# Optimization experiments

Hardware: AMD Instinct MI355X
Metric: run time of the kernel (lower is better)

The kernel has to match this reference:

```python
import jax, jax.numpy as jnp
import numpy as np

# ---- static config (mirrors GaussianLSS __init__) ----
ORF_H, ORF_W = 256, 704
FC, FH, FW = 128, 32, 88
D_ST, D_END, D_STEP = 4.0, 45.0, 1.0
OUT_C = 128
ERROR_TOL = 1.0
OPACITY_THR = 0.05
XB = (-50.0, 50.0, 1.0)
YB = (-50.0, 50.0, 1.0)
BEV_H = int(round((YB[1] - YB[0]) / YB[2]))
BEV_W = int(round((XB[1] - XB[0]) / XB[2]))
DS = np.arange(D_ST, D_END, D_STEP, dtype=np.float32)
D = DS.shape[0]  # 41
BN_EPS = 1e-3
CHUNK = 512      # gaussians composited per scan step (16896 = 33*512)
B, NCAM = 1, 6


def make_frustum():
    ds = jnp.broadcast_to(jnp.asarray(DS)[:, None, None], (D, FH, FW))
    xs = jnp.broadcast_to(jnp.linspace(0.0, ORF_W - 1.0, FW)[None, None, :], (D, FH, FW))
    ys = jnp.broadcast_to(jnp.linspace(0.0, ORF_H - 1.0, FH)[None, :, None], (D, FH, FW))
    return jnp.stack([xs, ys, ds], -1)  # [D,FH,FW,3]


def get_geometry(rots, trans, intrins, post_rots, post_trans):
    fr = make_frustum()
    pts = fr[None, None] - post_trans[:, :, None, None, None, :]
    pts = jnp.einsum('bnij,bndhwj->bndhwi', jnp.linalg.inv(post_rots), pts)
    pts = jnp.concatenate([pts[..., :2] * pts[..., 2:3], pts[..., 2:3]], -1)
    comb = jnp.einsum('bnij,bnjk->bnik', rots, jnp.linalg.inv(intrins))
    pts = jnp.einsum('bnij,bndhwj->bndhwi', comb, pts) + trans[:, :, None, None, None, :]
    return pts  # [B,N,D,FH,FW,3] ego-frame frustum points


def conv2d(x, w, b, pad):
    y = jax.lax.conv_general_dilated(x, w, (1, 1), [(pad, pad), (pad, pad)],
                                     dimension_numbers=('NCHW', 'OIHW', 'NCHW'))
    return y + b[None, :, None, None]


def bnorm(x, g, bt, m, v):
    s = (g / jnp.sqrt(v + BN_EPS))[None, :, None, None]
    return (x - m[None, :, None, None]) * s + bt[None, :, None, None]


def splat(means, cov6, colors, ops, valid_in):
    # Differentiable BEV gaussian rasterization (3DGS math, orthographic BEV camera,
    # all depths equal -> compositing in stable gaussian-index order).
    H, W = BEV_H, BEV_W
    sh, sw = H / 2.0, W / 2.0  # h/h_meters with FoV=2 (BEVCamera)
    my = -sh * means[:, 1] + H / 2.0  # pixel row (full_proj_transform row 0)
    mx = -sw * means[:, 0] + W / 2.0  # pixel col (row 1)
    a = sh * sh * cov6[:, 3] + 0.3    # 2D cov = J Sigma_xy J^T, +0.3 low-pass as in 3DGS
    c = sw * sw * cov6[:, 0] + 0.3
    b = sh * sw * cov6[:, 1]
    det = a * c - b * b
    valid = valid_in & (det > 0)
    inv_det = jnp.where(det > 0, 1.0 / det, 0.0)
    cA, cB, cC = c * inv_det, -b * inv_det, a * inv_det
    pi = jnp.repeat(jnp.arange(H, dtype=jnp.float32), W)  # [P] pixel rows
    pj = jnp.tile(jnp.arange(W, dtype=jnp.float32), H)    # [P] pixel cols
    G = means.shape[0]
    nchunk = G // CHUNK
    resh = lambda x: x.reshape((nchunk, CHUNK) + x.shape[1:])
    chunks = (resh(my), resh(mx), resh(cA), resh(cB), resh(cC),
              resh(ops), resh(valid), resh(colors))

    def body(carry, ch):
        logT, acc = carry
        my_c, mx_c, A, Bc, Cc, op_c, val_c, col_c = ch
        dI = pi[None, :] - my_c[:, None]                     # [Gc,P]
        dJ = pj[None, :] - mx_c[:, None]
        q = A[:, None] * dI * dI + 2.0 * Bc[:, None] * dI * dJ + Cc[:, None] * dJ * dJ
        alpha = jnp.minimum(0.99, op_c[:, None] * jnp.exp(-0.5 * q))
        alpha = jnp.where(val_c[:, None] & (q >= 0) & (alpha >= 1.0 / 255.0), alpha, 0.0)
        log1m = jnp.log1p(-alpha)
        cum = jnp.cumsum(log1m, axis=0)
        T = jnp.exp(logT[None, :] + cum - log1m)             # transmittance before each gaussian
        acc = acc + jnp.einsum('gp,gc->pc', alpha * T, col_c)
        return (logT + cum[-1], acc), None

    P = H * W
    init = (jnp.zeros((P,), jnp.float32), jnp.zeros((P, colors.shape[1]), jnp.float32))
    (_, acc), _ = jax.lax.scan(jax.checkpoint(body), init, chunks)
    return acc.reshape(H, W, -1).transpose(2, 0, 1)  # [C,H,W], bg is zeros


def _forward(cam2ego_rot, cam2ego_trans, cam_intrins, post_cam2ego_rot, post_cam2ego_trans,
             img_feats, conv1_w, conv1_b, bn1_g, bn1_b, bn1_m, bn1_v,
             conv2_w, conv2_b, bn2_g, bn2_b, bn2_m, bn2_v, conv3_w, conv3_b):
    geom = get_geometry(cam2ego_rot, cam2ego_trans, cam_intrins, post_cam2ego_rot, post_cam2ego_trans)
    b, n = img_feats.shape[:2]
    x = img_feats.reshape(b * n, FC, FH, FW)
    x = jax.nn.relu(bnorm(conv2d(x, conv1_w, conv1_b, 1), bn1_g, bn1_b, bn1_m, bn1_v))
    x = jax.nn.relu(bnorm(conv2d(x, conv2_w, conv2_b, 1), bn2_g, bn2_b, bn2_m, bn2_v))
    x = conv2d(x, conv3_w, conv3_b, 0)
    depth_prob = jax.nn.softmax(x[:, :D], axis=1).reshape(b, n, D, FH, FW)
    opac = jax.nn.sigmoid(x[:, D:D + 1]).reshape(b, n, FH, FW)
    feats = x[:, D + 1:].reshape(b, n, OUT_C, FH, FW)
    # per-pixel gaussian moments of the depth distribution (compute_gaussian)
    means = jnp.einsum('bndhw,bndhwi->bnhwi', depth_prob, geom)
    delta = means[:, :, None] - geom                                       # [B,N,D,FH,FW,3]
    cov = jnp.einsum('bndhw,bndhwi,bndhwj->bnhwij', depth_prob, delta, delta) * (ERROR_TOL ** 2 / 9.0)
    center = jnp.array([(XB[0] + XB[1]) / 2.0, (YB[0] + YB[1]) / 2.0, 0.0], jnp.float32)
    scale = jnp.array([2.0 / (XB[1] - XB[0]), 2.0 / (YB[1] - YB[0]), 1.0], jnp.float32)
    m_n = (means - center) * scale
    cov_n = cov * (scale[:, None] * scale[None, :])
    cov6 = jnp.stack([cov_n[..., 0, 0], cov_n[..., 0, 1], cov_n[..., 0, 2],
                      cov_n[..., 1, 1], cov_n[..., 1, 2], cov_n[..., 2, 2]], -1)
    g = n * FH * FW
    colors = feats.transpose(0, 1, 3, 4, 2).reshape(b, g, OUT_C)
    m_n = m_n.reshape(b, g, 3)
    cov6 = cov6.reshape(b, g, 6)
    ops = opac.reshape(b, g)
    mask = ops > OPACITY_THR  # opacity filtering == zero contribution, order preserved
    bev = jax.vmap(splat)(m_n, cov6, colors, ops, mask)                    # [B,C,H,W]
    num_gaussians = mask.astype(jnp.float32).sum(-1).mean()
    return bev, num_gaussians


def setup_inputs():
    key = jax.random.key(0)
    ks = jax.random.split(key, 8)
    # camera-to-ego rotations: cam->ego axis permutation composed with per-camera yaw
    yaw = np.linspace(0.0, 2.0 * np.pi, NCAM, endpoint=False).astype(np.float32)
    cz, sz = np.cos(yaw), np.sin(yaw)
    rotz = np.zeros((NCAM, 3, 3), np.float32)
    rotz[:, 0, 0] = cz; rotz[:, 0, 1] = -sz
    rotz[:, 1, 0] = sz; rotz[:, 1, 1] = cz
    rotz[:, 2, 2] = 1.0
    perm = np.array([[0.0, 0.0, 1.0], [-1.0, 0.0, 0.0], [0.0, -1.0, 0.0]], np.float32)
    rots = np.einsum('nij,jk->nik', rotz, perm)
    cam2ego_rot = jnp.asarray(np.broadcast_to(rots, (B, NCAM, 3, 3)).copy())
    cam2ego_trans = jax.random.normal(ks[0], (B, NCAM, 3), jnp.float32)
    K = np.array([[600.0, 0.0, ORF_W / 2.0], [0.0, 600.0, ORF_H / 2.0], [0.0, 0.0, 1.0]], np.float32)
    cam_intrins = jnp.asarray(np.broadcast_to(K, (B, NCAM, 3, 3)).copy())
    post_cam2ego_rot = jnp.broadcast_to(jnp.eye(3, dtype=jnp.float32), (B, NCAM, 3, 3)) + jnp.zeros((B, NCAM, 3, 3), jnp.float32)
    post_cam2ego_trans = jnp.zeros((B, NCAM, 3), jnp.float32)
    img_feats = jax.random.normal(ks[1], (B, NCAM, FC, FH, FW), jnp.float32)
    def conv_init(k, o, i, kh, kw):
        return jax.random.normal(k, (o, i, kh, kw), jnp.float32) * (1.0 / np.sqrt(i * kh * kw))
    return dict(cam2ego_rot=cam2ego_rot, cam2ego_trans=cam2ego_trans, cam_intrins=cam_intrins,
                post_cam2ego_rot=post_cam2ego_rot, post_cam2ego_trans=post_cam2ego_trans,
                img_feats=img_feats,
                conv1_w=conv_init(ks[2], FC, FC, 3, 3), conv1_b=jnp.zeros((FC,), jnp.float32),
                bn1_g=jnp.ones((FC,), jnp.float32), bn1_b=jnp.zeros((FC,), jnp.float32),
                bn1_m=jnp.zeros((FC,), jnp.float32), bn1_v=jnp.ones((FC,), jnp.float32),
                conv2_w=conv_init(ks[3], FC, FC, 3, 3), conv2_b=jnp.zeros((FC,), jnp.float32),
                bn2_g=jnp.ones((FC,), jnp.float32), bn2_b=jnp.zeros((FC,), jnp.float32),
                bn2_m=jnp.zeros((FC,), jnp.float32), bn2_v=jnp.ones((FC,), jnp.float32),
                conv3_w=conv_init(ks[4], OUT_C + D + 1, FC, 1, 1),
                conv3_b=jax.random.normal(ks[5], (OUT_C + D + 1,), jnp.float32) * 0.1)


def reference(cam2ego_rot, cam2ego_trans, cam_intrins, post_cam2ego_rot, post_cam2ego_trans,
              img_feats, conv1_w, conv1_b, bn1_g, bn1_b, bn1_m, bn1_v,
              conv2_w, conv2_b, bn2_g, bn2_b, bn2_m, bn2_v, conv3_w, conv3_b):
    return _forward(cam2ego_rot, cam2ego_trans, cam_intrins, post_cam2ego_rot, post_cam2ego_trans,
                    img_feats, conv1_w, conv1_b, bn1_g, bn1_b, bn1_m, bn1_v,
                    conv2_w, conv2_b, bn2_g, bn2_b, bn2_m, bn2_v, conv3_w, conv3_b)
```

## Files before the change

### kernel.cpp

```cpp
#include <hip/hip_runtime.h>

#define NCAM 6
#define FC   128
#define FH_  32
#define FW_  88
#define NPIX (FH_*FW_)
#define PH   34
#define PW   92
#define PPIX (PH*PW)
#define ND   41
#define X3D  42
#define OUTC 128
#define GTOT (NCAM*NPIX)
#define BEVH 100
#define BEVW 100
#define NPXB (BEVH*BEVW)
#define NTILE 25
#define NWORD 264
#define WCAP  70000
#define CSIZE 64
#define CBLK  2048

#define SZA     (NCAM*FC*PPIX)
#define WS_CAM  0
#define WS_A    256
#define WS_RB   (WS_A  + SZA)
#define WS_X3   (WS_RB + SZA)
#define WS_GS   (WS_X3 + NCAM*X3D*NPIX)
#define WS_WL   (WS_GS + GTOT*8)
#define WS_BASE (WS_WL + WCAP)

__device__ inline void inv3x3(const float* m, float* o) {
    float a=m[0],b=m[1],c=m[2],d=m[3],e=m[4],f=m[5],g=m[6],h=m[7],i=m[8];
    float A=e*i-f*h, B=c*h-b*i, C=b*f-c*e;
    float Dd=f*g-d*i, E=a*i-c*g, F=c*d-a*f;
    float Gg=d*h-e*g, H=b*g-a*h, I=a*e-b*d;
    float r = 1.0f/(a*A + b*Dd + c*Gg);
    o[0]=A*r; o[1]=B*r; o[2]=C*r; o[3]=Dd*r; o[4]=E*r; o[5]=F*r;
    o[6]=Gg*r; o[7]=H*r; o[8]=I*r;
}

__global__ void cam_consts_kernel(const float* __restrict__ rot, const float* __restrict__ tr,
                                  const float* __restrict__ intr, const float* __restrict__ prot,
                                  const float* __restrict__ ptr_, float* __restrict__ cam) {
    int n = threadIdx.x;
    if (n >= NCAM) return;
    float M1[9], Ki[9];
    inv3x3(prot + n*9, M1);
    inv3x3(intr + n*9, Ki);
    const float* R = rot + n*9;
    float* c = cam + n*24;
    for (int i=0;i<9;i++) c[i] = M1[i];
    for (int i=0;i<3;i++) c[9+i] = ptr_[n*3+i];
    for (int i=0;i<3;i++)
        for (int j=0;j<3;j++)
            c[12+i*3+j] = R[i*3+0]*Ki[0+j] + R[i*3+1]*Ki[3+j] + R[i*3+2]*Ki[6+j];
    for (int i=0;i<3;i++) c[21+i] = tr[n*3+i];
}

__global__ __launch_bounds__(256) void pad_input_kernel(const float* __restrict__ src,
                                                        float* __restrict__ dst) {
    int idx = blockIdx.x*256 + threadIdx.x;
    int plane = idx / NPIX, px = idx - plane*NPIX;
    int y = px / FW_, x = px - y*FW_;
    dst[(size_t)plane*PPIX + (y+1)*PW + (x+1)] = src[idx];
}

__global__ __launch_bounds__(256) void conv3x3_pf_kernel(
        const float* __restrict__ in, float* __restrict__ out, const float* __restrict__ w,
        const float* __restrict__ cb, const float* __restrict__ bg, const float* __restrict__ bb,
        const float* __restrict__ bm, const float* __restrict__ bv) {
    const int n   = blockIdx.x;
    const int co0 = blockIdx.y * 4;
    const int qid = blockIdx.z * 256 + threadIdx.x;
    if (qid >= 704) return;
    const int y = qid / 22, x0 = (qid - y*22) * 4;
    float scale[4], shift[4];
    #pragma unroll
    for (int c=0;c<4;c++) {
        float s = bg[co0+c] * rsqrtf(bv[co0+c] + 1e-3f);
        scale[c] = s;
        shift[c] = (cb[co0+c] - bm[co0+c]) * s + bb[co0+c];
    }
    float acc[4][4] = {};
    const float* ip = in + (size_t)n*FC*PPIX + y*PW + x0;
    const float* wb = w + (size_t)co0*FC*9;
    float4 p4[3]; float2 p2[3];
    #pragma unroll
    for (int r=0;r<3;r++) {
        p4[r] = *(const float4*)(ip + r*PW);
        p2[r] = *(const float2*)(ip + r*PW + 4);
    }
    for (int ci=0; ci<FC; ++ci) {
        float v[3][6];
        #pragma unroll
        for (int r=0;r<3;r++) {
            v[r][0]=p4[r].x; v[r][1]=p4[r].y; v[r][2]=p4[r].z; v[r][3]=p4[r].w;
            v[r][4]=p2[r].x; v[r][5]=p2[r].y;
        }
        if (ci + 1 < FC) {
            const float* ipn = ip + PPIX;
            #pragma unroll
            for (int r=0;r<3;r++) {
                p4[r] = *(const float4*)(ipn + r*PW);
                p2[r] = *(const float2*)(ipn + r*PW + 4);
            }
        }
        #pragma unroll
        for (int c=0;c<4;c++) {
            const float* wr = wb + (size_t)c*FC*9 + ci*9;
            float w00=wr[0],w01=wr[1],w02=wr[2],w10=wr[3],w11=wr[4],
                  w12=wr[5],w20=wr[6],w21=wr[7],w22=wr[8];
            #pragma unroll
            for (int p=0;p<4;p++) {
                float a = acc[c][p];
                a = fmaf(w00, v[0][p], a); a = fmaf(w01, v[0][p+1], a); a = fmaf(w02, v[0][p+2], a);
                a = fmaf(w10, v[1][p], a); a = fmaf(w11, v[1][p+1], a); a = fmaf(w12, v[1][p+2], a);
                a = fmaf(w20, v[2][p], a); a = fmaf(w21, v[2][p+1], a); a = fmaf(w22, v[2][p+2], a);
                acc[c][p] = a;
            }
        }
        ip += PPIX;
    }
    const int po = (y+1)*PW + (x0+1);
    #pragma unroll
    for (int c=0;c<4;c++) {
        float* op = out + ((size_t)n*FC + co0 + c)*PPIX + po;
        #pragma unroll
        for (int p=0;p<4;p++)
            op[p] = fmaxf(fmaf(acc[c][p], scale[c], shift[c]), 0.0f);
    }
}

__global__ __launch_bounds__(256) void conv1x1_kernel(const float* __restrict__ in,
        float* __restrict__ x3d, float* __restrict__ colors,
        const float* __restrict__ w, const float* __restrict__ b) {
    const int n   = blockIdx.x;
    const int px  = blockIdx.y * 256 + threadIdx.x;
    const int co0 = blockIdx.z * 8;
    const int y   = px / FW_, x = px - y*FW_;
    const int pp  = (y+1)*PW + (x+1);
    const float* wr[8];
    float acc[8];
    #pragma unroll
    for (int k=0;k<8;k++) {
        int co = min(co0 + k, 169);
        wr[k]  = w + (size_t)co*FC;
        acc[k] = b[co];
    }
    const float* ip = in + (size_t)n*FC*PPIX + pp;
    #pragma unroll 4
    for (int ci=0; ci<FC; ++ci) {
        float v = ip[(size_t)ci*PPIX];
        #pragma unroll
        for (int k=0;k<8;k++) acc[k] = fmaf(wr[k][ci], v, acc[k]);
    }
    #pragma unroll
    for (int k=0;k<8;k++) {
        int co = co0 + k;
        if (co < X3D)
            x3d[((size_t)n*X3D + co)*NPIX + px] = acc[k];
        else if (co < 170)
            colors[(((size_t)(n*NPIX + px)) << 7) + (co - X3D)] = acc[k];
    }
}

__global__ __launch_bounds__(256) void moments_kernel(const float* __restrict__ x3,
        const float* __restrict__ cam, float* __restrict__ gauss, float* __restrict__ ng) {
    int gi = blockIdx.x*256 + threadIdx.x;
    int n  = gi / NPIX;
    int p  = gi - n*NPIX;
    int h  = p / FW_, xp = p - h*FW_;
    const float* cc = cam + n*24;
    float u = xp * (703.0f/87.0f);
    float v = h  * (255.0f/31.0f);
    float fx = u - cc[9], fy = v - cc[10], fz = -cc[11];
    float p0x = cc[0]*fx + cc[1]*fy + cc[2]*fz;
    float p0y = cc[3]*fx + cc[4]*fy + cc[5]*fz;
    float p0z = cc[6]*fx + cc[7]*fy + cc[8]*fz;
    const float* lg = x3 + (size_t)n*X3D*NPIX + p;

    float mxl = -1e30f;
    for (int d=0; d<ND; ++d) mxl = fmaxf(mxl, lg[(size_t)d*NPIX]);
    float s=0.f, sgx=0.f, sgy=0.f;
    for (int d=0; d<ND; ++d) {
        float e  = __expf(lg[(size_t)d*NPIX] - mxl);
        float dz = 4.0f + (float)d;
        float pz = p0z + dz*cc[8];
        float px = (p0x + dz*cc[2]) * pz;
        float py = (p0y + dz*cc[5]) * pz;
        float gx = cc[12]*px + cc[13]*py + cc[14]*pz + cc[21];
        float gy = cc[15]*px + cc[16]*py + cc[17]*pz + cc[22];
        s += e; sgx += e*gx; sgy += e*gy;
    }
    float inv_s = 1.0f/s;
    float mex = sgx*inv_s, mey = sgy*inv_s;
    float cxx=0.f, cxy=0.f, cyy=0.f;
    for (int d=0; d<ND; ++d) {
        float e  = __expf(lg[(size_t)d*NPIX] - mxl);
        float dz = 4.0f + (float)d;
        float pz = p0z + dz*cc[8];
        float px = (p0x + dz*cc[2]) * pz;
        float py = (p0y + dz*cc[5]) * pz;
        float gx = cc[12]*px + cc[13]*py + cc[14]*pz + cc[21];
        float gy = cc[15]*px + cc[16]*py + cc[17]*pz + cc[22];
        float dxv = gx - mex, dyv = gy - mey;
        cxx += e*dxv*dxv; cxy += e*dxv*dyv; cyy += e*dyv*dyv;
    }
    const float k9 = inv_s * (1.0f/9.0f);
    cxx *= k9; cxy *= k9; cyy *= k9;

    float lo = lg[(size_t)ND*NPIX];
    float op = 1.0f/(1.0f + __expf(-lo));
    bool mask = op > 0.05f;

    const float SC = 0.02f, SH = 50.0f, SW = 50.0f;
    float my = -SH*(mey*SC) + 50.0f;
    float mx = -SW*(mex*SC) + 50.0f;
    float a  = SH*SH*(cyy*SC*SC) + 0.3f;
    float b  = SH*SW*(cxy*SC*SC);
    float c  = SW*SW*(cxx*SC*SC) + 0.3f;
    float det = a*c - b*b;
    bool valid = mask && (det > 0.0f);
    float A, B2, C, qm, ri, rj;
    if (valid) {
        float idet = 1.0f/det;
        A = c*idet; B2 = -2.0f*b*idet; C = a*idet;
        qm = 2.0f*__logf(255.0f*op);
        ri = sqrtf(qm*a); rj = sqrtf(qm*c);
    } else { A=B2=C=0.f; qm=-1.0f; ri=-1e30f; rj=-1e30f; }
    float* gp = gauss + (size_t)gi*8;
    gp[0]=my; gp[1]=mx; gp[2]=A; gp[3]=B2; gp[4]=C; gp[5]=qm; gp[6]=ri; gp[7]=rj;

    unsigned long long bal = __ballot(mask);
    if ((threadIdx.x & 63) == 0) atomicAdd(ng, (float)__popcll(bal));
}

__global__ __launch_bounds__(256) void build_masks_kernel(const float* __restrict__ gauss,
        unsigned long long* __restrict__ masks) {
    const int g = blockIdx.x*256 + threadIdx.x;
    const float4 g0 = *(const float4*)(gauss + ((size_t)g << 3));
    const float4 g1 = *(const float4*)(gauss + ((size_t)g << 3) + 4);
    if (g1.y < 0.0f) return;
    const float my = g0.x, mx = g0.y, A = g0.z, B = 0.5f*g0.w, C = g1.x, qm = g1.y, ri = g1.z;
    const float invC = 1.0f / C;
    const float k2 = C*A - B*B;
    int ti0 = max(0, (int)floorf((my - ri) * 0.25f));
    int ti1 = min(NTILE-1, (int)floorf((my + ri) * 0.25f));
    const int wi = g >> 6;
    const unsigned long long bit = 1ull << (g & 63);
    for (int ti = ti0; ti <= ti1; ++ti) {
        float jmn = 1e30f, jmx = -1e30f;
        #pragma unroll
        for (int r = 0; r < 4; ++r) {
            int i = 4*ti + r;
            if (i < 0 || i > 99) continue;
            float di = (float)i - my;
            float disc = C*qm - k2*di*di;
            if (disc < 0.0f) continue;
            float sd = sqrtf(disc);
            float jc = -B*di;
            jmn = fminf(jmn, (jc - sd)*invC + mx);
            jmx = fmaxf(jmx, (jc + sd)*invC + mx);
        }
        if (jmx < jmn) continue;
        int jl = max(0, (int)ceilf(jmn));
        int jh = min(99, (int)floorf(jmx));
        if (jl > jh) continue;
        for (int tj = (jl >> 2); tj <= (jh >> 2); ++tj)
            atomicOr(&masks[(size_t)(ti*NTILE + tj)*NWORD + wi], bit);
    }
}

__global__ __launch_bounds__(256) void cnt_kernel(const unsigned long long* __restrict__ masks,
                                                  int* __restrict__ cnt) {
    __shared__ int sc;
    const int tile = blockIdx.x, t = threadIdx.x;
    if (t == 0) sc = 0;
    __syncthreads();
    if (t < NWORD) atomicAdd(&sc, __popcll(masks[(size_t)tile*NWORD + t]));
    __syncthreads();
    if (t == 0) cnt[tile] = sc;
}

__global__ __launch_bounds__(640) void scan_kernel(const int* __restrict__ cnt,
        int* __restrict__ off, int* __restrict__ choff, int* __restrict__ nwork) {
    __shared__ int wsum[16], wsum2[16];
    const int t = threadIdx.x;
    const int lane = t & 63, wv = t >> 6;
    int c  = (t < NTILE*NTILE) ? cnt[t] : 0;
    int ch = (c + CSIZE-1) >> 6;
    int v = c, v2 = ch;
    #pragma unroll
    for (int o = 1; o < 64; o <<= 1) {
        int u  = __shfl_up(v,  (unsigned)o, 64);
        int u2 = __shfl_up(v2, (unsigned)o, 64);
        if (lane >= o) { v += u; v2 += u2; }
    }
    if (lane == 63) { wsum[wv] = v; wsum2[wv] = v2; }
    __syncthreads();
    int pre = 0, pre2 = 0;
    for (int w2 = 0; w2 < wv; ++w2) { pre += wsum[w2]; pre2 += wsum2[w2]; }
    int inc = v + pre, inc2 = v2 + pre2;
    if (t < NTILE*NTILE) { off[t] = inc - c; choff[t] = inc2 - ch; }
    if (t == NTILE*NTILE - 1) {
        off[NTILE*NTILE] = inc;
        choff[NTILE*NTILE] = inc2;
        nwork[0] = (inc2 > WCAP) ? WCAP : inc2;
    }
}

__global__ __launch_bounds__(256) void fill_kernel(const unsigned long long* __restrict__ masks,
        const int* __restrict__ cnt, const int* __restrict__ off, const int* __restrict__ choff,
        unsigned short* __restrict__ list, int* __restrict__ wl) {
    __shared__ unsigned long long sw[NWORD];
    __shared__ int wpre[NWORD];
    const int tile = blockIdx.x, t = threadIdx.x;
    if (t < NWORD) sw[t] = masks[(size_t)tile*NWORD + t];
    __syncthreads();
    if (t == 0) {
        int run = 0;
        for (int w2 = 0; w2 < NWORD; ++w2) { wpre[w2] = run; run += __popcll(sw[w2]); }
    }
    __syncthreads();
    if (t < NWORD) {
        unsigned long long m = sw[t];
        int pos = off[tile] + wpre[t], base = t << 6;
        while (m) { int b = __builtin_ctzll(m); m &= m - 1; list[pos++] = (unsigned short)(base + b); }
    }
    int nch = (cnt[tile] + CSIZE-1)/CSIZE;
    int c0 = choff[tile];
    if (t < nch && c0 + t < WCAP) wl[c0 + t] = (tile << 9) | t;
}

__device__ inline float eval_alpha(const float4 g0, const float4 g1, float fi, float fj) {
    float dI = fi - g0.x, dJ = fj - g0.y;
    float q = dI*(g0.z*dI + g0.w*dJ) + g1.x*dJ*dJ;
    if (q < 0.0f || q > g1.y) return 0.0f;
    return fminf(0.99f, 0.003921568627f * __expf(0.5f*(g1.y - q)));
}

__global__ __launch_bounds__(256) void chunk_sums_kernel(const float* __restrict__ gauss,
        const unsigned short* __restrict__ list, const int* __restrict__ cnt,
        const int* __restrict__ off, const int* __restrict__ wl, const int* __restrict__ nwork,
        float* __restrict__ base) {
    const int nw = nwork[0];
    const int t = threadIdx.x;
    const int px = t & 15, kg = t >> 4;
    __shared__ unsigned short slist[CSIZE];
    __shared__ float red[16][17];
    for (int e = blockIdx.x; e < nw; e += gridDim.x) {
        int v = wl[e], tile = v >> 9, c = v & 511;
        int hbase = off[tile] + (c << 6);
        int nh = min(CSIZE, cnt[tile] - (c << 6));
        if (t < nh) slist[t] = list[hbase + t];
        __syncthreads();
        const int i0 = (tile / NTILE) * 4, j0 = (tile % NTILE) * 4;
        const float fi = (float)(i0 + (px >> 2)), fj = (float)(j0 + (px & 3));
        float s = 0.0f;
        for (int k = kg; k < nh; k += 16) {
            int g = slist[k];
            float4 g0 = *(const float4*)(gauss + ((size_t)g << 3));
            float4 g1 = *(const float4*)(gauss + ((size_t)g << 3) + 4);
            float a = eval_alpha(g0, g1, fi, fj);
            if (a > 0.0f) s += __logf(1.0f - a);
        }
        red[kg][px] = s;
        __syncthreads();
        if (t < 16) {
            float acc = 0.0f;
            #pragma unroll
            for (int k2 = 0; k2 < 16; ++k2) acc += red[k2][t];
            base[(size_t)e*16 + t] = acc;
        }
        __syncthreads();
    }
}

__global__ __launch_bounds__(256) void chunk_prefix_kernel(const int* __restrict__ choff,
                                                           float* __restrict__ base) {
    __shared__ float part[16][17];
    const int tile = blockIdx.x, t = threadIdx.x;
    const int c0 = choff[tile], nch = choff[tile+1] - c0;
    if (nch == 0) return;
    const int px = t & 15, cg = t >> 4;
    const int L16 = (nch + 15) >> 4;
    const int a0 = cg*L16, a1 = min(nch, a0 + L16);
    float s = 0.0f;
    for (int c = a0; c < a1; ++c) s += base[(size_t)(c0 + c)*16 + px];
    part[cg][px] = s;
    __syncthreads();
    if (t < 16) {
        float run = 0.0f;
        #pragma unroll
        for (int k = 0; k < 16; ++k) { float tmp = part[k][t]; part[k][t] = run; run += tmp; }
    }
    __syncthreads();
    float run = part[cg][px];
    for (int c = a0; c < a1; ++c) {
        size_t idx = (size_t)(c0 + c)*16 + px;
        float tmp = base[idx];
        base[idx] = run;
        run += tmp;
    }
}

__global__ __launch_bounds__(256) void composite_kernel(const float* __restrict__ gauss,
        const float* __restrict__ colors, const unsigned short* __restrict__ list,
        const int* __restrict__ cnt, const int* __restrict__ off, const int* __restrict__ wl,
        const int* __restrict__ nwork, const float* __restrict__ base, float* __restrict__ out) {
    const int nw = nwork[0];
    const int t = threadIdx.x;
    const int lane = t & 63;
    const int e_px = t >> 4, e_kg = t & 15;
    const int a_cs4 = t & 31, a_pxq = t >> 5;
    __shared__ unsigned short slist[2][CSIZE];
    __shared__ float s_w[CSIZE][17];
    const int per = (nw + CBLK - 1) / CBLK;
    int e0 = blockIdx.x * per;
    if (e0 >= nw) return;
    int e1 = min(nw, e0 + per);

    float4 acc0 = make_float4(0.f,0.f,0.f,0.f);
    float4 acc1 = make_float4(0.f,0.f,0.f,0.f);
    int cur_tile = wl[e0] >> 9;
    int cur_i0 = (cur_tile / NTILE) * 4, cur_j0 = (cur_tile % NTILE) * 4;

    int buf = 0;
    {
        int v = wl[e0], tl = v >> 9, c = v & 511;
        int nh0 = min(CSIZE, cnt[tl] - (c << 6));
        if (t < nh0) slist[0][t] = list[off[tl] + (c << 6) + t];
    }

    for (int e = e0; e < e1; ++e) {
        int v = wl[e], tile = v >> 9, c = v & 511;
        if (tile != cur_tile) {
            const int pix0 = (cur_i0 + (a_pxq >> 2)) * BEVW + cur_j0 + (a_pxq & 3);
            const int pix1 = pix0 + 2 * BEVW;
            float* op = out + (size_t)(a_cs4 << 2) * NPXB;
            atomicAdd(op + 0*NPXB + pix0, acc0.x); atomicAdd(op + 1*NPXB + pix0, acc0.y);
            atomicAdd(op + 2*NPXB + pix0, acc0.z); atomicAdd(op + 3*NPXB + pix0, acc0.w);
            atomicAdd(op + 0*NPXB + pix1, acc1.x); atomicAdd(op + 1*NPXB + pix1, acc1.y);
            atomicAdd(op + 2*NPXB + pix1, acc1.z); atomicAdd(op + 3*NPXB + pix1, acc1.w);
            acc0 = make_float4(0.f,0.f,0.f,0.f);
            acc1 = make_float4(0.f,0.f,0.f,0.f);
            cur_tile = tile;
            cur_i0 = (tile / NTILE) * 4; cur_j0 = (tile % NTILE) * 4;
        }
        const int nh = min(CSIZE, cnt[cur_tile] - (c << 6));
        __syncthreads();
        if (e + 1 < e1) {
            int v2 = wl[e+1], tl2 = v2 >> 9, c2 = v2 & 511;
            int nh2 = min(CSIZE, cnt[tl2] - (c2 << 6));
            if (t < nh2) slist[buf^1][t] = list[off[tl2] + (c2 << 6) + t];
        }
        {
            const float fi = (float)(cur_i0 + (e_px >> 2)), fj = (float)(cur_j0 + (e_px & 3));
            const int k0 = e_kg << 2;
            float a4[4]; float lsum = 0.0f;
            #pragma unroll
            for (int i = 0; i < 4; ++i) {
                int k = k0 + i;
                float a = 0.0f;
                if (k < nh) {
                    int g = slist[buf][k];
                    float4 g0 = *(const float4*)(gauss + ((size_t)g << 3));
                    float4 g1 = *(const float4*)(gauss + ((size_t)g << 3) + 4);
                    a = eval_alpha(g0, g1, fi, fj);
                }
                a4[i] = a;
                if (a > 0.0f) lsum += __logf(1.0f - a);
            }
            float s = lsum;
            #pragma unroll
            for (int o = 1; o < 16; o <<= 1) {
                float u = __shfl_up(s, (unsigned)o, 64);
                if ((lane & 15) >= o) s += u;
            }
            float T = __expf(base[(size_t)e*16 + e_px] + (s - lsum));
            #pragma unroll
            for (int i = 0; i < 4; ++i) {
                float wv = a4[i] * T; T -= wv;
                s_w[k0 + i][e_px] = wv;
            }
        }
        __syncthreads();
        const float* colbase = colors;
        if (nh == CSIZE) {
            #pragma unroll 8
            for (int k = 0; k < CSIZE; ++k) {
                int g = slist[buf][k];
                float w0 = s_w[k][a_pxq];
                float w1 = s_w[k][a_pxq + 8];
                float4 cl = *(const float4*)(colbase + ((size_t)g << 7) + (a_cs4 << 2));
                acc0.x = fmaf(w0, cl.x, acc0.x); acc0.y = fmaf(w0, cl.y, acc0.y);
                acc0.z = fmaf(w0, cl.z, acc0.z); acc0.w = fmaf(w0, cl.w, acc0.w);
                acc1.x = fmaf(w1, cl.x, acc1.x); acc1.y = fmaf(w1, cl.y, acc1.y);
                acc1.z = fmaf(w1, cl.z, acc1.z); acc1.w = fmaf(w1, cl.w, acc1.w);
            }
        } else {
            #pragma unroll 4
            for (int k = 0; k < nh; ++k) {
                int g = slist[buf][k];
                float w0 = s_w[k][a_pxq];
                float w1 = s_w[k][a_pxq + 8];
                float4 cl = *(const float4*)(colbase + ((size_t)g << 7) + (a_cs4 << 2));
                acc0.x = fmaf(w0, cl.x, acc0.x); acc0.y = fmaf(w0, cl.y, acc0.y);
                acc0.z = fmaf(w0, cl.z, acc0.z); acc0.w = fmaf(w0, cl.w, acc0.w);
                acc1.x = fmaf(w1, cl.x, acc1.x); acc1.y = fmaf(w1, cl.y, acc1.y);
                acc1.z = fmaf(w1, cl.z, acc1.z); acc1.w = fmaf(w1, cl.w, acc1.w);
            }
        }
        buf ^= 1;
    }
    const int pix0 = (cur_i0 + (a_pxq >> 2)) * BEVW + cur_j0 + (a_pxq & 3);
    const int pix1 = pix0 + 2 * BEVW;
    float* op = out + (size_t)(a_cs4 << 2) * NPXB;
    atomicAdd(op + 0*NPXB + pix0, acc0.x); atomicAdd(op + 1*NPXB + pix0, acc0.y);
    atomicAdd(op + 2*NPXB + pix0, acc0.z); atomicAdd(op + 3*NPXB + pix0, acc0.w);
    atomicAdd(op + 0*NPXB + pix1, acc1.x); atomicAdd(op + 1*NPXB + pix1, acc1.y);
    atomicAdd(op + 2*NPXB + pix1, acc1.z); atomicAdd(op + 3*NPXB + pix1, acc1.w);
}

extern "C" void kernel_launch(void* const* d_in, const int* in_sizes, int n_in,
                              void* d_out, int out_size, void* d_ws, size_t ws_size,
                              hipStream_t stream) {
    const float* rot  = (const float*)d_in[0];
    const float* tr   = (const float*)d_in[1];
    const float* intr = (const float*)d_in[2];
    const float* prot = (const float*)d_in[3];
    const float* ptr_ = (const float*)d_in[4];
    const float* img  = (const float*)d_in[5];
    const float* c1w  = (const float*)d_in[6];  const float* c1b = (const float*)d_in[7];
    const float* b1g  = (const float*)d_in[8];  const float* b1b = (const float*)d_in[9];
    const float* b1m  = (const float*)d_in[10]; const float* b1v = (const float*)d_in[11];
    const float* c2w  = (const float*)d_in[12]; const float* c2b = (const float*)d_in[13];
    const float* b2g  = (const float*)d_in[14]; const float* b2b = (const float*)d_in[15];
    const float* b2m  = (const float*)d_in[16]; const float* b2v = (const float*)d_in[17];
    const float* c3w  = (const float*)d_in[18]; const float* c3b = (const float*)d_in[19];
    float* out = (float*)d_out;
    float* ws  = (float*)d_ws;
    float* CAM = ws + WS_CAM;
    float* RA  = ws + WS_A;
    float* RB  = ws + WS_RB;
    float* X3B = ws + WS_X3;
    float* GS  = ws + WS_GS;
    int*   WL  = (int*)(ws + WS_WL);
    float* BASE = ws + WS_BASE;
    unsigned long long* MASKS = (unsigned long long*)X3B;
    int* AUXI = (int*)(ws + WS_X3 + 330000);
    int* CNT = AUXI;
    int* OFF = AUXI + 640;
    int* CHOFF = AUXI + 1280;
    int* NWORK = AUXI + 1920;
    unsigned short* LIST = (unsigned short*)RA;
    float* COL = RB;
    float* ngp = out + (size_t)NPXB*OUTC;

    cam_consts_kernel<<<1, 64, 0, stream>>>(rot, tr, intr, prot, ptr_, CAM);
    (void)hipMemsetAsync(RA, 0, (size_t)SZA*sizeof(float), stream);
    (void)hipMemsetAsync(RB, 0, (size_t)SZA*sizeof(float), stream);
    pad_input_kernel<<<NCAM*FC*NPIX/256, 256, 0, stream>>>(img, RA);
    conv3x3_pf_kernel<<<dim3(NCAM,32,3), 256, 0, stream>>>(RA, RB, c1w, c1b, b1g, b1b, b1m, b1v);
    conv3x3_pf_kernel<<<dim3(NCAM,32,3), 256, 0, stream>>>(RB, RA, c2w, c2b, b2g, b2b, b2m, b2v);
    conv1x1_kernel<<<dim3(NCAM,11,22), 256, 0, stream>>>(RA, X3B, COL, c3w, c3b);
    (void)hipMemsetAsync(ngp, 0, sizeof(float), stream);
    (void)hipMemsetAsync(out, 0, (size_t)NPXB*OUTC*sizeof(float), stream);
    moments_kernel<<<GTOT/256, 256, 0, stream>>>(X3B, CAM, GS, ngp);
    (void)hipMemsetAsync(MASKS, 0, (size_t)NTILE*NTILE*NWORD*sizeof(unsigned long long), stream);
    build_masks_kernel<<<GTOT/256, 256, 0, stream>>>(GS, MASKS);
    cnt_kernel<<<NTILE*NTILE, 256, 0, stream>>>(MASKS, CNT);
    scan_kernel<<<1, 640, 0, stream>>>(CNT, OFF, CHOFF, NWORK);
    fill_kernel<<<NTILE*NTILE, 256, 0, stream>>>(MASKS, CNT, OFF, CHOFF, LIST, WL);
    chunk_sums_kernel<<<8192, 256, 0, stream>>>(GS, LIST, CNT, OFF, WL, NWORK, BASE);
    chunk_prefix_kernel<<<NTILE*NTILE, 256, 0, stream>>>(CHOFF, BASE);
    composite_kernel<<<CBLK, 256, 0, stream>>>(GS, COL, LIST, CNT, OFF, WL, NWORK, BASE, out);
}
```

Before: 487.4 us.

## Fuse setup kernels and memsets, cache logits, use product transmittance

Merges camera-constant computation and mask building into the moments kernel, and folds all workspace/output zeroing into the padding kernel, removing several launches and memsets. Logits are kept in registers so exp is computed once per depth bin. Chunk transmittance sums switch from log-sum to direct products with per-wave work items and shuffle reductions, and conv3x3 uses 128-thread blocks. Products may underflow differently than log sums, and masks now alias the chunk-base buffer.

New measurement: 473.2 us. 1.03x faster.

```diff
diff --git a/kernel.cpp b/kernel.cpp
--- a/kernel.cpp
+++ b/kernel.cpp
@@ -17,6 +17,7 @@
 #define NPXB (BEVH*BEVW)
 #define NTILE 25
 #define NWORD 264
+#define NMASKW (NTILE*NTILE*NWORD)
 #define WCAP  70000
 #define CSIZE 64
 #define CBLK  2048
@@ -40,39 +41,30 @@
     o[6]=Gg*r; o[7]=H*r; o[8]=I*r;
 }
 
-__global__ void cam_consts_kernel(const float* __restrict__ rot, const float* __restrict__ tr,
-                                  const float* __restrict__ intr, const float* __restrict__ prot,
-                                  const float* __restrict__ ptr_, float* __restrict__ cam) {
-    int n = threadIdx.x;
-    if (n >= NCAM) return;
-    float M1[9], Ki[9];
-    inv3x3(prot + n*9, M1);
-    inv3x3(intr + n*9, Ki);
-    const float* R = rot + n*9;
-    float* c = cam + n*24;
-    for (int i=0;i<9;i++) c[i] = M1[i];
-    for (int i=0;i<3;i++) c[9+i] = ptr_[n*3+i];
-    for (int i=0;i<3;i++)
-        for (int j=0;j<3;j++)
-            c[12+i*3+j] = R[i*3+0]*Ki[0+j] + R[i*3+1]*Ki[3+j] + R[i*3+2]*Ki[6+j];
-    for (int i=0;i<3;i++) c[21+i] = tr[n*3+i];
-}
-
 __global__ __launch_bounds__(256) void pad_input_kernel(const float* __restrict__ src,
-                                                        float* __restrict__ dst) {
+        float* __restrict__ dst, float* __restrict__ rb,
+        float* __restrict__ outp, unsigned long long* __restrict__ masks) {
     int idx = blockIdx.x*256 + threadIdx.x;
-    int plane = idx / NPIX, px = idx - plane*NPIX;
-    int y = px / FW_, x = px - y*FW_;
-    dst[(size_t)plane*PPIX + (y+1)*PW + (x+1)] = src[idx];
-}
-
-__global__ __launch_bounds__(256) void conv3x3_pf_kernel(
+    if (idx < NMASKW) masks[idx] = 0ull;
+    if (idx <= NPXB*OUTC) outp[idx] = 0.0f;
+    if (idx >= NCAM*FC*PPIX) return;
+    int plane = idx / PPIX, pp = idx - plane*PPIX;
+    int y = pp / PW, x = pp - y*PW;
+    bool interior = (y >= 1 && y <= FH_ && x >= 1 && x <= FW_);
+    float v = 0.0f;
+    if (interior)
+        v = src[(size_t)plane*NPIX + (y-1)*FW_ + (x-1)];
+    dst[idx] = v;
+    if (!interior) rb[idx] = 0.0f;
+}
+
+__global__ __launch_bounds__(128) void conv3x3_pf_kernel(
         const float* __restrict__ in, float* __restrict__ out, const float* __restrict__ w,
         const float* __restrict__ cb, const float* __restrict__ bg, const float* __restrict__ bb,
         const float* __restrict__ bm, const float* __restrict__ bv) {
     const int n   = blockIdx.x;
     const int co0 = blockIdx.y * 4;
-    const int qid = blockIdx.z * 256 + threadIdx.x;
+    const int qid = blockIdx.z * 128 + threadIdx.x;
     if (qid >= 704) return;
     const int y = qid / 22, x0 = (qid - y*22) * 4;
     float scale[4], shift[4];
@@ -165,13 +157,34 @@
     }
 }
 
-__global__ __launch_bounds__(256) void moments_kernel(const float* __restrict__ x3,
-        const float* __restrict__ cam, float* __restrict__ gauss, float* __restrict__ ng) {
-    int gi = blockIdx.x*256 + threadIdx.x;
-    int n  = gi / NPIX;
-    int p  = gi - n*NPIX;
-    int h  = p / FW_, xp = p - h*FW_;
-    const float* cc = cam + n*24;
+__global__ __launch_bounds__(256) void moments_masks_kernel(const float* __restrict__ x3,
+        const float* __restrict__ rot, const float* __restrict__ tr,
+        const float* __restrict__ intr, const float* __restrict__ prot,
+        const float* __restrict__ ptr_, float* __restrict__ gauss,
+        unsigned long long* __restrict__ masks, float* __restrict__ ng) {
+    __shared__ float cc[24];
+    const int n = blockIdx.x / 11;
+    if (threadIdx.x == 0) {
+        float M1[9], Ki[9];
+        inv3x3(prot + n*9, M1);
+        inv3x3(intr + n*9, Ki);
+        const float* R = rot + n*9;
+        #pragma unroll
+        for (int i=0;i<9;i++) cc[i] = M1[i];
+        #pragma unroll
+        for (int i=0;i<3;i++) cc[9+i] = ptr_[n*3+i];
+        #pragma unroll
+        for (int i=0;i<3;i++)
+            #pragma unroll
+            for (int j=0;j<3;j++)
+                cc[12+i*3+j] = R[i*3+0]*Ki[0+j] + R[i*3+1]*Ki[3+j] + R[i*3+2]*Ki[6+j];
+        #pragma unroll
+        for (int i=0;i<3;i++) cc[21+i] = tr[n*3+i];
+    }
+    __syncthreads();
+    const int gi = blockIdx.x*256 + threadIdx.x;
+    const int p  = gi - n*NPIX;
+    const int h  = p / FW_, xp = p - h*FW_;
     float u = xp * (703.0f/87.0f);
     float v = h  * (255.0f/31.0f);
     float fx = u - cc[9], fy = v - cc[10], fz = -cc[11];
@@ -180,11 +193,19 @@
     float p0z = cc[6]*fx + cc[7]*fy + cc[8]*fz;
     const float* lg = x3 + (size_t)n*X3D*NPIX + p;
 
+    float lgv[ND];
+    #pragma unroll
+    for (int d=0; d<ND; ++d) lgv[d] = lg[(size_t)d*NPIX];
+
     float mxl = -1e30f;
-    for (int d=0; d<ND; ++d) mxl = fmaxf(mxl, lg[(size_t)d*NPIX]);
+    #pragma unroll
+    for (int d=0; d<ND; ++d) mxl = fmaxf(mxl, lgv[d]);
+
     float s=0.f, sgx=0.f, sgy=0.f;
+    #pragma unroll
     for (int d=0; d<ND; ++d) {
-        float e  = __expf(lg[(size_t)d*NPIX] - mxl);
+        float e  = __expf(lgv[d] - mxl);
+        lgv[d] = e;
         float dz = 4.0f + (float)d;
         float pz = p0z + dz*cc[8];
         float px = (p0x + dz*cc[2]) * pz;
@@ -196,8 +217,9 @@
     float inv_s = 1.0f/s;
     float mex = sgx*inv_s, mey = sgy*inv_s;
     float cxx=0.f, cxy=0.f, cyy=0.f;
+    #pragma unroll
     for (int d=0; d<ND; ++d) {
-        float e  = __expf(lg[(size_t)d*NPIX] - mxl);
+        float e  = lgv[d];
         float dz = 4.0f + (float)d;
         float pz = p0z + dz*cc[8];
         float px = (p0x + dz*cc[2]) * pz;
@@ -234,21 +256,15 @@
 
     unsigned long long bal = __ballot(mask);
     if ((threadIdx.x & 63) == 0) atomicAdd(ng, (float)__popcll(bal));
-}
-
-__global__ __launch_bounds__(256) void build_masks_kernel(const float* __restrict__ gauss,
-        unsigned long long* __restrict__ masks) {
-    const int g = blockIdx.x*256 + threadIdx.x;
-    const float4 g0 = *(const float4*)(gauss + ((size_t)g << 3));
-    const float4 g1 = *(const float4*)(gauss + ((size_t)g << 3) + 4);
-    if (g1.y < 0.0f) return;
-    const float my = g0.x, mx = g0.y, A = g0.z, B = 0.5f*g0.w, C = g1.x, qm = g1.y, ri = g1.z;
+
+    if (!valid) return;
+    const float B = 0.5f*B2;
     const float invC = 1.0f / C;
     const float k2 = C*A - B*B;
     int ti0 = max(0, (int)floorf((my - ri) * 0.25f));
     int ti1 = min(NTILE-1, (int)floorf((my + ri) * 0.25f));
-    const int wi = g >> 6;
-    const unsigned long long bit = 1ull << (g & 63);
+    const int wi = gi >> 6;
+    const unsigned long long bit = 1ull << (gi & 63);
     for (int ti = ti0; ti <= ti1; ++ti) {
         float jmn = 1e30f, jmx = -1e30f;
         #pragma unroll
@@ -345,35 +361,27 @@
         const int* __restrict__ off, const int* __restrict__ wl, const int* __restrict__ nwork,
         float* __restrict__ base) {
     const int nw = nwork[0];
-    const int t = threadIdx.x;
-    const int px = t & 15, kg = t >> 4;
-    __shared__ unsigned short slist[CSIZE];
-    __shared__ float red[16][17];
-    for (int e = blockIdx.x; e < nw; e += gridDim.x) {
+    const int lane = threadIdx.x & 63;
+    const int wid  = (blockIdx.x * 256 + threadIdx.x) >> 6;
+    const int nwv  = (gridDim.x * 256) >> 6;
+    const int px = lane & 15, kg = lane >> 4;
+    for (int e = wid; e < nw; e += nwv) {
         int v = wl[e], tile = v >> 9, c = v & 511;
         int hbase = off[tile] + (c << 6);
         int nh = min(CSIZE, cnt[tile] - (c << 6));
-        if (t < nh) slist[t] = list[hbase + t];
-        __syncthreads();
         const int i0 = (tile / NTILE) * 4, j0 = (tile % NTILE) * 4;
         const float fi = (float)(i0 + (px >> 2)), fj = (float)(j0 + (px & 3));
-        float s = 0.0f;
-        for (int k = kg; k < nh; k += 16) {
-            int g = slist[k];
+        float s = 1.0f;
+        for (int k = kg; k < nh; k += 4) {
+            int g = list[hbase + k];
             float4 g0 = *(const float4*)(gauss + ((size_t)g << 3));
             float4 g1 = *(const float4*)(gauss + ((size_t)g << 3) + 4);
             float a = eval_alpha(g0, g1, fi, fj);
-            if (a > 0.0f) s += __logf(1.0f - a);
-        }
-        red[kg][px] = s;
-        __syncthreads();
-        if (t < 16) {
-            float acc = 0.0f;
-            #pragma unroll
-            for (int k2 = 0; k2 < 16; ++k2) acc += red[k2][t];
-            base[(size_t)e*16 + t] = acc;
-        }
-        __syncthreads();
+            s *= (1.0f - a);
+        }
+        s *= __shfl_xor(s, 16, 64);
+        s *= __shfl_xor(s, 32, 64);
+        if (lane < 16) base[(size_t)e*16 + lane] = s;
     }
 }
 
@@ -386,14 +394,14 @@
     const int px = t & 15, cg = t >> 4;
     const int L16 = (nch + 15) >> 4;
     const int a0 = cg*L16, a1 = min(nch, a0 + L16);
-    float s = 0.0f;
-    for (int c = a0; c < a1; ++c) s += base[(size_t)(c0 + c)*16 + px];
+    float s = 1.0f;
+    for (int c = a0; c < a1; ++c) s *= base[(size_t)(c0 + c)*16 + px];
     part[cg][px] = s;
     __syncthreads();
     if (t < 16) {
-        float run = 0.0f;
-        #pragma unroll
-        for (int k = 0; k < 16; ++k) { float tmp = part[k][t]; part[k][t] = run; run += tmp; }
+        float run = 1.0f;
+        #pragma unroll
+        for (int k = 0; k < 16; ++k) { float tmp = part[k][t]; part[k][t] = run; run *= tmp; }
     }
     __syncthreads();
     float run = part[cg][px];
@@ -401,7 +409,7 @@
         size_t idx = (size_t)(c0 + c)*16 + px;
         float tmp = base[idx];
         base[idx] = run;
-        run += tmp;
+        run *= tmp;
     }
 }
 
@@ -458,7 +466,7 @@
         {
             const float fi = (float)(cur_i0 + (e_px >> 2)), fj = (float)(cur_j0 + (e_px & 3));
             const int k0 = e_kg << 2;
-            float a4[4]; float lsum = 0.0f;
+            float a4[4]; float p = 1.0f;
             #pragma unroll
             for (int i = 0; i < 4; ++i) {
                 int k = k0 + i;
@@ -470,15 +478,16 @@
                     a = eval_alpha(g0, g1, fi, fj);
                 }
                 a4[i] = a;
-                if (a > 0.0f) lsum += __logf(1.0f - a);
-            }
-            float s = lsum;
+                p *= (1.0f - a);
+            }
+            float s = p;
             #pragma unroll
             for (int o = 1; o < 16; o <<= 1) {
                 float u = __shfl_up(s, (unsigned)o, 64);
-                if ((lane & 15) >= o) s += u;
-            }
-            float T = __expf(base[(size_t)e*16 + e_px] + (s - lsum));
+                if ((lane & 15) >= o) s *= u;
+            }
+            float ex = __shfl_up(s, 1u, 64);
+            float T = base[(size_t)e*16 + e_px] * (((lane & 15) == 0) ? 1.0f : ex);
             #pragma unroll
             for (int i = 0; i < 4; ++i) {
                 float wv = a4[i] * T; T -= wv;
@@ -541,14 +550,13 @@
     const float* c3w  = (const float*)d_in[18]; const float* c3b = (const float*)d_in[19];
     float* out = (float*)d_out;
     float* ws  = (float*)d_ws;
-    float* CAM = ws + WS_CAM;
     float* RA  = ws + WS_A;
     float* RB  = ws + WS_RB;
     float* X3B = ws + WS_X3;
     float* GS  = ws + WS_GS;
     int*   WL  = (int*)(ws + WS_WL);
     float* BASE = ws + WS_BASE;
-    unsigned long long* MASKS = (unsigned long long*)X3B;
+    unsigned long long* MASKS = (unsigned long long*)BASE;
     int* AUXI = (int*)(ws + WS_X3 + 330000);
     int* CNT = AUXI;
     int* OFF = AUXI + 640;
@@ -558,18 +566,12 @@
     float* COL = RB;
     float* ngp = out + (size_t)NPXB*OUTC;
 
-    cam_consts_kernel<<<1, 64, 0, stream>>>(rot, tr, intr, prot, ptr_, CAM);
-    (void)hipMemsetAsync(RA, 0, (size_t)SZA*sizeof(float), stream);
-    (void)hipMemsetAsync(RB, 0, (size_t)SZA*sizeof(float), stream);
-    pad_input_kernel<<<NCAM*FC*NPIX/256, 256, 0, stream>>>(img, RA);
-    conv3x3_pf_kernel<<<dim3(NCAM,32,3), 256, 0, stream>>>(RA, RB, c1w, c1b, b1g, b1b, b1m, b1v);
-    conv3x3_pf_kernel<<<dim3(NCAM,32,3), 256, 0, stream>>>(RB, RA, c2w, c2b, b2g, b2b, b2m, b2v);
+    pad_input_kernel<<<(NCAM*FC*PPIX + 255)/256, 256, 0, stream>>>(img, RA, RB, out, MASKS);
+    conv3x3_pf_kernel<<<dim3(NCAM,32,6), 128, 0, stream>>>(RA, RB, c1w, c1b, b1g, b1b, b1m, b1v);
+    conv3x3_pf_kernel<<<dim3(NCAM,32,6), 128, 0, stream>>>(RB, RA, c2w, c2b, b2g, b2b, b2m, b2v);
     conv1x1_kernel<<<dim3(NCAM,11,22), 256, 0, stream>>>(RA, X3B, COL, c3w, c3b);
-    (void)hipMemsetAsync(ngp, 0, sizeof(float), stream);
-    (void)hipMemsetAsync(out, 0, (size_t)NPXB*OUTC*sizeof(float), stream);
-    moments_kernel<<<GTOT/256, 256, 0, stream>>>(X3B, CAM, GS, ngp);
-    (void)hipMemsetAsync(MASKS, 0, (size_t)NTILE*NTILE*NWORD*sizeof(unsigned long long), stream);
-    build_masks_kernel<<<GTOT/256, 256, 0, stream>>>(GS, MASKS);
+    moments_masks_kernel<<<GTOT/256, 256, 0, stream>>>(X3B, rot, tr, intr, prot, ptr_,
+                                                       GS, MASKS, ngp);
     cnt_kernel<<<NTILE*NTILE, 256, 0, stream>>>(MASKS, CNT);
     scan_kernel<<<1, 640, 0, stream>>>(CNT, OFF, CHOFF, NWORK);
     fill_kernel<<<NTILE*NTILE, 256, 0, stream>>>(MASKS, CNT, OFF, CHOFF, LIST, WL);
```
